# Kernel tuning notes

Hardware: AMD Instinct MI355X
Metric: run time of the kernel (lower is better)

Reference implementation:

```python
import jax, jax.numpy as jnp
import numpy as np

B, N, D, H = 32, 2048, 1024, 16
HD = D // H


def setup_inputs() -> dict:
    key = jax.random.key(0)
    ks = jax.random.split(key, 12)
    s = 1.0 / np.sqrt(D)  # xavier-ish scale for square projections
    return {
        "z": jax.random.normal(ks[0], (B, N, D), dtype=jnp.float32),
        "mask": jax.random.bernoulli(ks[1], 0.9, (B, N)),
        "query": jax.random.normal(ks[2], (1, 1, D), dtype=jnp.float32) * s,
        "w_q": jax.random.normal(ks[3], (D, D), dtype=jnp.float32) * s,
        "w_k": jax.random.normal(ks[4], (D, D), dtype=jnp.float32) * s,
        "w_v": jax.random.normal(ks[5], (D, D), dtype=jnp.float32) * s,
        "b_q": jnp.zeros((D,), dtype=jnp.float32),
        "b_k": jnp.zeros((D,), dtype=jnp.float32),
        "b_v": jnp.zeros((D,), dtype=jnp.float32),
        "w_o": jax.random.normal(ks[6], (D, D), dtype=jnp.float32) * s,
        "b_o": jnp.zeros((D,), dtype=jnp.float32),
    }


def reference(z, mask, query, w_q, w_k, w_v, b_q, b_k, b_v, w_o, b_o):
    # mask: True = valid key. Guarantee at least one valid key per row
    # (torch code sets mask[b, 0] = True for all-False rows).
    all_false = ~jnp.any(mask, axis=1)                 # [B]
    valid = mask.at[:, 0].set(mask[:, 0] | all_false)  # [B, N]

    # Projections (PyTorch Linear: x @ W.T + b)
    q = (query @ w_q.T + b_q).reshape(H, HD)           # single shared query -> [H, HD]
    k = (z @ w_k.T + b_k).reshape(B, N, H, HD)
    v = (z @ w_v.T + b_v).reshape(B, N, H, HD)

    scale = 1.0 / jnp.sqrt(jnp.asarray(HD, dtype=z.dtype))
    scores = jnp.einsum('hd,bnhd->bhn', q, k) * scale  # [B, H, N]
    scores = jnp.where(valid[:, None, :], scores, -jnp.inf)
    attn = jax.nn.softmax(scores, axis=-1)             # [B, H, N]

    pooled = jnp.einsum('bhn,bnhd->bhd', attn, v).reshape(B, D)
    return pooled @ w_o.T + b_o                        # [B, D]
```

## Files before the change

### kernel.cpp

```cpp
#include <hip/hip_runtime.h>
#include <stdint.h>

#define B_ 32
#define N_ 2048
#define D_ 1024
#define H_ 16

typedef __attribute__((ext_vector_type(8))) short short8;
typedef __attribute__((ext_vector_type(4))) float f32x4;

__device__ __forceinline__ unsigned short f2bf(float x) {
    unsigned u = __float_as_uint(x);
    u += 0x7FFFu + ((u >> 16) & 1u);
    return (unsigned short)(u >> 16);
}
__device__ __forceinline__ float bfhi(unsigned u) { return __uint_as_float(u & 0xFFFF0000u); }
__device__ __forceinline__ float bflo(unsigned u) { return __uint_as_float(u << 16); }

__global__ __launch_bounds__(256) void gemv_k(const float* __restrict__ vec_base, int vdiv,
        const float* __restrict__ W, const float* __restrict__ bias,
        float* __restrict__ out, int nout, int mod) {
    __shared__ float vlds[1024];
    int bx = blockIdx.x, t = threadIdx.x;
    const float* vec = vec_base + (size_t)(bx / vdiv) * 1024;
    float* orow = out + (size_t)(bx / mod) * 1024;
    int j0 = (bx % mod) * nout;
    *(float4*)&vlds[4 * t] = *(const float4*)&vec[4 * t];
    __syncthreads();
    int w = t >> 6, l = t & 63;
    int per = nout >> 2;
    for (int s = 0; s < per; s++) {
        int j = j0 + w * per + s;
        const float4* Wr = (const float4*)(W + (size_t)j * 1024);
        float acc = 0.f;
        #pragma unroll
        for (int kk = 0; kk < 4; kk++) {
            float4 a = Wr[kk * 64 + l];
            float4 v = *(const float4*)&vlds[(kk * 64 + l) * 4];
            acc += a.x * v.x + a.y * v.y + a.z * v.z + a.w * v.w;
        }
        #pragma unroll
        for (int m = 32; m >= 1; m >>= 1) acc += __shfl_xor(acc, m, 64);
        if (l == 0) orow[j] = acc + bias[j];
    }
}

__global__ __launch_bounds__(256) void prep_k(const float* __restrict__ q,
        const float* __restrict__ wk, const int* __restrict__ mask,
        unsigned short* __restrict__ rAf, int* __restrict__ any_ws) {
    __shared__ float qh[64];
    __shared__ int wf[4];
    int bx = blockIdx.x, t = threadIdx.x;
    if (bx < 16) {
        int h = bx;
        if (t < 64) qh[t] = q[h * 64 + t];
        __syncthreads();
        float4 acc = make_float4(0.f, 0.f, 0.f, 0.f);
        const float4* wk4 = (const float4*)wk;
        for (int j = 0; j < 64; j++) {
            float qv = qh[j];
            float4 wv = wk4[(size_t)(h * 64 + j) * 256 + t];
            acc.x += qv * wv.x; acc.y += qv * wv.y;
            acc.z += qv * wv.z; acc.w += qv * wv.w;
        }
        const float scale = 0.125f;
        float av[4] = {acc.x * scale, acc.y * scale, acc.z * scale, acc.w * scale};
        #pragma unroll
        for (int dd = 0; dd < 4; dd++) {
            int d = 4 * t + dd;
            int i = d >> 5, g = (d >> 3) & 3, jj = d & 7;
            int lane = (g << 4) | h;
            rAf[(size_t)(i * 64 + lane) * 8 + jj] = f2bf(av[dd]);
        }
    } else {
        int b = bx - 16;
        int v = 0;
        for (int k = 0; k < 8; k++) v |= mask[b * N_ + k * 256 + t];
        unsigned long long bal = __ballot(v != 0);
        int w = t >> 6;
        if ((t & 63) == 0) wf[w] = (bal != 0ull) ? 1 : 0;
        __syncthreads();
        if (t == 0) any_ws[b] = wf[0] | wf[1] | wf[2] | wf[3];
    }
}

__global__ __launch_bounds__(256, 2) void main_k(const float* __restrict__ z,
        const int* __restrict__ mask, const int* __restrict__ any_ws,
        const unsigned short* __restrict__ rAf,
        unsigned short* __restrict__ ctx_ws, float* __restrict__ l_ws) {
    __shared__ unsigned short zt[16][1024];
    __shared__ float Cpart[4][16][16];
    __shared__ float E_lds[256];
    __shared__ float lred[256];
    int bx = blockIdx.x, t = threadIdx.x;
    int b = bx >> 5, c = bx & 31;
    int n0 = c * 64;
    int w = t >> 6, l = t & 63;
    int frow = l & 15, fquad = l >> 4;
    int eh = t & 15, en = t >> 4;
    int anyb = any_ws[b];
    const float4* zg4 = (const float4*)(z + (size_t)b * N_ * D_);
    const short8* rA8 = (const short8*)rAf;
    float4 ctx[16];
    #pragma unroll
    for (int h = 0; h < 16; h++) ctx[h] = make_float4(0.f, 0.f, 0.f, 0.f);
    float l_acc = 0.f;

    for (int it = 0; it < 4; it++) {
        int rbase = n0 + it * 16;
        #pragma unroll
        for (int k = 0; k < 16; k++) {
            float4 v = zg4[(size_t)(rbase + k) * 256 + t];
            ushort4 o;
            o.x = f2bf(v.x); o.y = f2bf(v.y); o.z = f2bf(v.z); o.w = f2bf(v.w);
            *(ushort4*)&zt[k][4 * t] = o;
        }
        __syncthreads();
        f32x4 acc = {0.f, 0.f, 0.f, 0.f};
        #pragma unroll
        for (int ib = 0; ib < 8; ib++) {
            int i = w * 8 + ib;
            short8 af = rA8[i * 64 + l];
            short8 bf = *(const short8*)&zt[frow][i * 32 + fquad * 8];
            acc = __builtin_amdgcn_mfma_f32_16x16x32_bf16(af, bf, acc, 0, 0, 0);
        }
        #pragma unroll
        for (int r = 0; r < 4; r++) Cpart[w][fquad * 4 + r][frow] = acc[r];
        __syncthreads();
        {
            float s = Cpart[0][eh][en] + Cpart[1][eh][en]
                    + Cpart[2][eh][en] + Cpart[3][eh][en];
            int gn = rbase + en;
            bool valid = (mask[b * N_ + gn] != 0) || (gn == 0 && anyb == 0);
            float e = valid ? __expf(s) : 0.f;
            E_lds[t] = e;
            l_acc += e;
        }
        __syncthreads();
        for (int r = 0; r < 16; r++) {
            float er[16];
            *(float4*)&er[0]  = *(const float4*)&E_lds[r * 16 + 0];
            *(float4*)&er[4]  = *(const float4*)&E_lds[r * 16 + 4];
            *(float4*)&er[8]  = *(const float4*)&E_lds[r * 16 + 8];
            *(float4*)&er[12] = *(const float4*)&E_lds[r * 16 + 12];
            uint2 p = *(const uint2*)&zt[r][4 * t];
            float z0 = bflo(p.x), z1 = bfhi(p.x), z2 = bflo(p.y), z3 = bfhi(p.y);
            #pragma unroll
            for (int h = 0; h < 16; h++) {
                float e = er[h];
                ctx[h].x += e * z0; ctx[h].y += e * z1;
                ctx[h].z += e * z2; ctx[h].w += e * z3;
            }
        }
        __syncthreads();
    }
    #pragma unroll
    for (int h = 0; h < 16; h++) {
        ushort4 o;
        o.x = f2bf(ctx[h].x); o.y = f2bf(ctx[h].y);
        o.z = f2bf(ctx[h].z); o.w = f2bf(ctx[h].w);
        *(ushort4*)&ctx_ws[((size_t)bx * 16 + h) * 1024 + 4 * t] = o;
    }
    lred[t] = l_acc;
    __syncthreads();
    if (t < 16) {
        float s = 0.f;
        #pragma unroll
        for (int ss = 0; ss < 16; ss++) s += lred[ss * 16 + t];
        l_ws[bx * 16 + t] = s;
    }
}

__global__ __launch_bounds__(256) void reduce_k(const unsigned short* __restrict__ ctx_ws,
        const float* __restrict__ l_ws, const float* __restrict__ z,
        float* __restrict__ ctxsum) {
    int o = blockIdx.x * 256 + threadIdx.x;
    int b = o >> 14, h = (o >> 10) & 15, d = o & 1023;
    float s = 0.f, L = 0.f;
    for (int c = 0; c < 32; c++) {
        int bx = b * 32 + c;
        unsigned short us = ctx_ws[((size_t)bx * 16 + h) * 1024 + d];
        s += bflo((unsigned)us);
        L += l_ws[bx * 16 + h];
    }
    float val;
    if (L > 0.f) val = s / L;
    else         val = z[((size_t)b * N_ + 0) * D_ + d];
    ctxsum[o] = val;
}

extern "C" void kernel_launch(void* const* d_in, const int* in_sizes, int n_in,
                              void* d_out, int out_size, void* d_ws, size_t ws_size,
                              hipStream_t stream) {
    const float* z     = (const float*)d_in[0];
    const int*   mask  = (const int*)d_in[1];
    const float* query = (const float*)d_in[2];
    const float* w_q   = (const float*)d_in[3];
    const float* w_k   = (const float*)d_in[4];
    const float* w_v   = (const float*)d_in[5];
    const float* b_q   = (const float*)d_in[6];
    const float* b_v   = (const float*)d_in[8];
    const float* w_o   = (const float*)d_in[9];
    const float* b_o   = (const float*)d_in[10];
    float* out = (float*)d_out;

    char* ws = (char*)d_ws;
    float*          q_ws   = (float*)(ws + 0);
    int*            any_ws = (int*)(ws + 4096);
    unsigned short* rAf    = (unsigned short*)(ws + 8192);
    float*          l_ws   = (float*)(ws + 40960);
    float*          ctxsum = (float*)(ws + 131072);
    float*          pooled = (float*)(ws + 2228224);
    unsigned short* ctx_ws = (unsigned short*)(ws + 4194304);

    gemv_k<<<64, 256, 0, stream>>>(query, 64, w_q, b_q, q_ws, 16, 64);
    prep_k<<<48, 256, 0, stream>>>(q_ws, w_k, mask, rAf, any_ws);
    main_k<<<1024, 256, 0, stream>>>(z, mask, any_ws, rAf, ctx_ws, l_ws);
    reduce_k<<<2048, 256, 0, stream>>>(ctx_ws, l_ws, z, ctxsum);
    gemv_k<<<512, 256, 0, stream>>>(ctxsum, 1, w_v, b_v, pooled, 64, 16);
    gemv_k<<<512, 256, 0, stream>>>(pooled, 16, w_o, b_o, out, 64, 16);
}
```

Measured before the change: 469.8 us.

## Double-buffer z tiles in main kernel and fuse reduction into w_v gemv

Main kernel now processes 128 rows per block with register prefetch of the next 16-row z tile overlapping the MFMA/accumulate work on the current LDS buffer. Partial contexts are written in fp32 and the cross-chunk reduction and normalization are fused into the w_v gemv, removing a kernel and a bf16 round trip. The q projection is folded into prep_k and the gemvs compute four outputs per pass. The added prefetch registers may raise register pressure and halve the block count.

New measurement: 733.2 us. +56.1%, slower.

```diff
diff --git a/kernel.cpp b/kernel.cpp
--- a/kernel.cpp
+++ b/kernel.cpp
@@ -17,51 +17,44 @@
 __device__ __forceinline__ float bfhi(unsigned u) { return __uint_as_float(u & 0xFFFF0000u); }
 __device__ __forceinline__ float bflo(unsigned u) { return __uint_as_float(u << 16); }
 
-__global__ __launch_bounds__(256) void gemv_k(const float* __restrict__ vec_base, int vdiv,
-        const float* __restrict__ W, const float* __restrict__ bias,
-        float* __restrict__ out, int nout, int mod) {
-    __shared__ float vlds[1024];
-    int bx = blockIdx.x, t = threadIdx.x;
-    const float* vec = vec_base + (size_t)(bx / vdiv) * 1024;
-    float* orow = out + (size_t)(bx / mod) * 1024;
-    int j0 = (bx % mod) * nout;
-    *(float4*)&vlds[4 * t] = *(const float4*)&vec[4 * t];
-    __syncthreads();
-    int w = t >> 6, l = t & 63;
-    int per = nout >> 2;
-    for (int s = 0; s < per; s++) {
-        int j = j0 + w * per + s;
-        const float4* Wr = (const float4*)(W + (size_t)j * 1024);
-        float acc = 0.f;
-        #pragma unroll
-        for (int kk = 0; kk < 4; kk++) {
-            float4 a = Wr[kk * 64 + l];
-            float4 v = *(const float4*)&vlds[(kk * 64 + l) * 4];
-            acc += a.x * v.x + a.y * v.y + a.z * v.z + a.w * v.w;
-        }
-        #pragma unroll
-        for (int m = 32; m >= 1; m >>= 1) acc += __shfl_xor(acc, m, 64);
-        if (l == 0) orow[j] = acc + bias[j];
-    }
-}
-
-__global__ __launch_bounds__(256) void prep_k(const float* __restrict__ q,
-        const float* __restrict__ wk, const int* __restrict__ mask,
+__global__ __launch_bounds__(256) void prep_k(const float* __restrict__ query,
+        const float* __restrict__ w_q, const float* __restrict__ b_q,
+        const float* __restrict__ w_k, const int* __restrict__ mask,
         unsigned short* __restrict__ rAf, int* __restrict__ any_ws) {
+    __shared__ __align__(16) float qv[1024];
+    __shared__ float qpart[64][4];
     __shared__ float qh[64];
     __shared__ int wf[4];
     int bx = blockIdx.x, t = threadIdx.x;
     if (bx < 16) {
         int h = bx;
-        if (t < 64) qh[t] = q[h * 64 + t];
+        *(float4*)&qv[4 * t] = *(const float4*)&query[4 * t];
+        __syncthreads();
+        {
+            int j = t >> 2, qr = t & 3;
+            const float4* wq4 = (const float4*)w_q;
+            const float4* qv4 = (const float4*)qv;
+            float a = 0.f;
+            #pragma unroll 4
+            for (int kk = 0; kk < 64; kk++) {
+                float4 wv = wq4[(size_t)(h * 64 + j) * 256 + qr * 64 + kk];
+                float4 vv = qv4[qr * 64 + kk];
+                a += wv.x * vv.x + wv.y * vv.y + wv.z * vv.z + wv.w * vv.w;
+            }
+            qpart[j][qr] = a;
+        }
+        __syncthreads();
+        if (t < 64)
+            qh[t] = qpart[t][0] + qpart[t][1] + qpart[t][2] + qpart[t][3] + b_q[h * 64 + t];
         __syncthreads();
         float4 acc = make_float4(0.f, 0.f, 0.f, 0.f);
-        const float4* wk4 = (const float4*)wk;
-        for (int j = 0; j < 64; j++) {
-            float qv = qh[j];
-            float4 wv = wk4[(size_t)(h * 64 + j) * 256 + t];
-            acc.x += qv * wv.x; acc.y += qv * wv.y;
-            acc.z += qv * wv.z; acc.w += qv * wv.w;
+        const float4* wk4 = (const float4*)w_k;
+        #pragma unroll 4
+        for (int jj = 0; jj < 64; jj++) {
+            float qq = qh[jj];
+            float4 wv = wk4[(size_t)(h * 64 + jj) * 256 + t];
+            acc.x += qq * wv.x; acc.y += qq * wv.y;
+            acc.z += qq * wv.z; acc.w += qq * wv.w;
         }
         const float scale = 0.125f;
         float av[4] = {acc.x * scale, acc.y * scale, acc.z * scale, acc.w * scale};
@@ -87,14 +80,14 @@
 __global__ __launch_bounds__(256, 2) void main_k(const float* __restrict__ z,
         const int* __restrict__ mask, const int* __restrict__ any_ws,
         const unsigned short* __restrict__ rAf,
-        unsigned short* __restrict__ ctx_ws, float* __restrict__ l_ws) {
-    __shared__ unsigned short zt[16][1024];
+        float* __restrict__ part, float* __restrict__ l_part) {
+    __shared__ __align__(16) unsigned short zt[2][16][1040];
     __shared__ float Cpart[4][16][16];
     __shared__ float E_lds[256];
     __shared__ float lred[256];
     int bx = blockIdx.x, t = threadIdx.x;
-    int b = bx >> 5, c = bx & 31;
-    int n0 = c * 64;
+    int b = bx >> 4, c = bx & 15;
+    int n0 = c * 128;
     int w = t >> 6, l = t & 63;
     int frow = l & 15, fquad = l >> 4;
     int eh = t & 15, en = t >> 4;
@@ -106,31 +99,40 @@
     for (int h = 0; h < 16; h++) ctx[h] = make_float4(0.f, 0.f, 0.f, 0.f);
     float l_acc = 0.f;
 
-    for (int it = 0; it < 4; it++) {
-        int rbase = n0 + it * 16;
-        #pragma unroll
-        for (int k = 0; k < 16; k++) {
-            float4 v = zg4[(size_t)(rbase + k) * 256 + t];
-            ushort4 o;
-            o.x = f2bf(v.x); o.y = f2bf(v.y); o.z = f2bf(v.z); o.w = f2bf(v.w);
-            *(ushort4*)&zt[k][4 * t] = o;
-        }
-        __syncthreads();
+    float4 vv[16];
+    #pragma unroll
+    for (int k = 0; k < 16; k++) vv[k] = zg4[(size_t)(n0 + k) * 256 + t];
+    #pragma unroll
+    for (int k = 0; k < 16; k++) {
+        ushort4 o;
+        o.x = f2bf(vv[k].x); o.y = f2bf(vv[k].y);
+        o.z = f2bf(vv[k].z); o.w = f2bf(vv[k].w);
+        *(ushort4*)&zt[0][k][4 * t] = o;
+    }
+
+    for (int it = 0; it < 8; it++) {
+        int p = it & 1;
+        __syncthreads();
+        if (it < 7) {
+            int rb = n0 + (it + 1) * 16;
+            #pragma unroll
+            for (int k = 0; k < 16; k++) vv[k] = zg4[(size_t)(rb + k) * 256 + t];
+        }
         f32x4 acc = {0.f, 0.f, 0.f, 0.f};
         #pragma unroll
         for (int ib = 0; ib < 8; ib++) {
             int i = w * 8 + ib;
             short8 af = rA8[i * 64 + l];
-            short8 bf = *(const short8*)&zt[frow][i * 32 + fquad * 8];
+            short8 bf = *(const short8*)&zt[p][frow][i * 32 + fquad * 8];
             acc = __builtin_amdgcn_mfma_f32_16x16x32_bf16(af, bf, acc, 0, 0, 0);
         }
         #pragma unroll
         for (int r = 0; r < 4; r++) Cpart[w][fquad * 4 + r][frow] = acc[r];
         __syncthreads();
         {
+            int gn = n0 + it * 16 + en;
             float s = Cpart[0][eh][en] + Cpart[1][eh][en]
                     + Cpart[2][eh][en] + Cpart[3][eh][en];
-            int gn = rbase + en;
             bool valid = (mask[b * N_ + gn] != 0) || (gn == 0 && anyb == 0);
             float e = valid ? __expf(s) : 0.f;
             E_lds[t] = e;
@@ -143,8 +145,8 @@
             *(float4*)&er[4]  = *(const float4*)&E_lds[r * 16 + 4];
             *(float4*)&er[8]  = *(const float4*)&E_lds[r * 16 + 8];
             *(float4*)&er[12] = *(const float4*)&E_lds[r * 16 + 12];
-            uint2 p = *(const uint2*)&zt[r][4 * t];
-            float z0 = bflo(p.x), z1 = bfhi(p.x), z2 = bflo(p.y), z3 = bfhi(p.y);
+            uint2 pz = *(const uint2*)&zt[p][r][4 * t];
+            float z0 = bflo(pz.x), z1 = bfhi(pz.x), z2 = bflo(pz.y), z3 = bfhi(pz.y);
             #pragma unroll
             for (int h = 0; h < 16; h++) {
                 float e = er[h];
@@ -152,41 +154,121 @@
                 ctx[h].z += e * z2; ctx[h].w += e * z3;
             }
         }
-        __syncthreads();
-    }
-    #pragma unroll
-    for (int h = 0; h < 16; h++) {
-        ushort4 o;
-        o.x = f2bf(ctx[h].x); o.y = f2bf(ctx[h].y);
-        o.z = f2bf(ctx[h].z); o.w = f2bf(ctx[h].w);
-        *(ushort4*)&ctx_ws[((size_t)bx * 16 + h) * 1024 + 4 * t] = o;
-    }
+        if (it < 7) {
+            #pragma unroll
+            for (int k = 0; k < 16; k++) {
+                ushort4 o;
+                o.x = f2bf(vv[k].x); o.y = f2bf(vv[k].y);
+                o.z = f2bf(vv[k].z); o.w = f2bf(vv[k].w);
+                *(ushort4*)&zt[p ^ 1][k][4 * t] = o;
+            }
+        }
+    }
+    #pragma unroll
+    for (int h = 0; h < 16; h++)
+        *(float4*)&part[((size_t)bx * 16 + h) * 1024 + 4 * t] = ctx[h];
     lred[t] = l_acc;
     __syncthreads();
     if (t < 16) {
         float s = 0.f;
         #pragma unroll
-        for (int ss = 0; ss < 16; ss++) s += lred[ss * 16 + t];
-        l_ws[bx * 16 + t] = s;
-    }
-}
-
-__global__ __launch_bounds__(256) void reduce_k(const unsigned short* __restrict__ ctx_ws,
-        const float* __restrict__ l_ws, const float* __restrict__ z,
-        float* __restrict__ ctxsum) {
-    int o = blockIdx.x * 256 + threadIdx.x;
-    int b = o >> 14, h = (o >> 10) & 15, d = o & 1023;
-    float s = 0.f, L = 0.f;
-    for (int c = 0; c < 32; c++) {
-        int bx = b * 32 + c;
-        unsigned short us = ctx_ws[((size_t)bx * 16 + h) * 1024 + d];
-        s += bflo((unsigned)us);
-        L += l_ws[bx * 16 + h];
-    }
-    float val;
-    if (L > 0.f) val = s / L;
-    else         val = z[((size_t)b * N_ + 0) * D_ + d];
-    ctxsum[o] = val;
+        for (int g = 0; g < 16; g++) s += lred[g * 16 + t];
+        l_part[bx * 16 + t] = s;
+    }
+}
+
+__global__ __launch_bounds__(256) void gemv_wv_k(const float* __restrict__ part,
+        const float* __restrict__ l_part, const float* __restrict__ w_v,
+        const float* __restrict__ b_v, float* __restrict__ pooled) {
+    __shared__ __align__(16) float vlds[1024];
+    int bx = blockIdx.x, t = threadIdx.x;
+    int b = bx >> 4, h = bx & 15;
+    float L = 0.f;
+    #pragma unroll
+    for (int cc = 0; cc < 16; cc++) L += l_part[(b * 16 + cc) * 16 + h];
+    float rL = 1.f / L;
+    float sx = 0.f, sy = 0.f, sz = 0.f, sw = 0.f;
+    #pragma unroll
+    for (int cc = 0; cc < 16; cc++) {
+        const float4* p4 = (const float4*)&part[(((size_t)(b * 16 + cc)) * 16 + h) * 1024];
+        float4 v = p4[t];
+        sx += v.x; sy += v.y; sz += v.z; sw += v.w;
+    }
+    float4 o = make_float4(sx * rL, sy * rL, sz * rL, sw * rL);
+    *(float4*)&vlds[4 * t] = o;
+    __syncthreads();
+    int w = t >> 6, l = t & 63;
+    const float4* v4 = (const float4*)vlds;
+    float* orow = pooled + (size_t)b * 1024;
+    #pragma unroll
+    for (int s0 = 0; s0 < 16; s0 += 4) {
+        int jb = h * 64 + w * 16 + s0;
+        float a0 = 0.f, a1 = 0.f, a2 = 0.f, a3 = 0.f;
+        #pragma unroll
+        for (int kk = 0; kk < 4; kk++) {
+            float4 v = v4[kk * 64 + l];
+            float4 w0 = *(const float4*)&w_v[(size_t)(jb + 0) * 1024 + (kk * 64 + l) * 4];
+            float4 w1 = *(const float4*)&w_v[(size_t)(jb + 1) * 1024 + (kk * 64 + l) * 4];
+            float4 w2 = *(const float4*)&w_v[(size_t)(jb + 2) * 1024 + (kk * 64 + l) * 4];
+            float4 w3 = *(const float4*)&w_v[(size_t)(jb + 3) * 1024 + (kk * 64 + l) * 4];
+            a0 += w0.x * v.x + w0.y * v.y + w0.z * v.z + w0.w * v.w;
+            a1 += w1.x * v.x + w1.y * v.y + w1.z * v.z + w1.w * v.w;
+            a2 += w2.x * v.x + w2.y * v.y + w2.z * v.z + w2.w * v.w;
+            a3 += w3.x * v.x + w3.y * v.y + w3.z * v.z + w3.w * v.w;
+        }
+        #pragma unroll
+        for (int m = 32; m >= 1; m >>= 1) {
+            a0 += __shfl_xor(a0, m, 64); a1 += __shfl_xor(a1, m, 64);
+            a2 += __shfl_xor(a2, m, 64); a3 += __shfl_xor(a3, m, 64);
+        }
+        if (l == 0) {
+            orow[jb + 0] = a0 + b_v[jb + 0];
+            orow[jb + 1] = a1 + b_v[jb + 1];
+            orow[jb + 2] = a2 + b_v[jb + 2];
+            orow[jb + 3] = a3 + b_v[jb + 3];
+        }
+    }
+}
+
+__global__ __launch_bounds__(256) void gemv_wo_k(const float* __restrict__ pooled,
+        const float* __restrict__ w_o, const float* __restrict__ b_o,
+        float* __restrict__ out) {
+    __shared__ __align__(16) float vlds[1024];
+    int bx = blockIdx.x, t = threadIdx.x;
+    int b = bx >> 4, q = bx & 15;
+    *(float4*)&vlds[4 * t] = *(const float4*)&pooled[(size_t)b * 1024 + 4 * t];
+    __syncthreads();
+    int w = t >> 6, l = t & 63;
+    const float4* v4 = (const float4*)vlds;
+    float* orow = out + (size_t)b * 1024;
+    #pragma unroll
+    for (int s0 = 0; s0 < 16; s0 += 4) {
+        int jb = q * 64 + w * 16 + s0;
+        float a0 = 0.f, a1 = 0.f, a2 = 0.f, a3 = 0.f;
+        #pragma unroll
+        for (int kk = 0; kk < 4; kk++) {
+            float4 v = v4[kk * 64 + l];
+            float4 w0 = *(const float4*)&w_o[(size_t)(jb + 0) * 1024 + (kk * 64 + l) * 4];
+            float4 w1 = *(const float4*)&w_o[(size_t)(jb + 1) * 1024 + (kk * 64 + l) * 4];
+            float4 w2 = *(const float4*)&w_o[(size_t)(jb + 2) * 1024 + (kk * 64 + l) * 4];
+            float4 w3 = *(const float4*)&w_o[(size_t)(jb + 3) * 1024 + (kk * 64 + l) * 4];
+            a0 += w0.x * v.x + w0.y * v.y + w0.z * v.z + w0.w * v.w;
+            a1 += w1.x * v.x + w1.y * v.y + w1.z * v.z + w1.w * v.w;
+            a2 += w2.x * v.x + w2.y * v.y + w2.z * v.z + w2.w * v.w;
+            a3 += w3.x * v.x + w3.y * v.y + w3.z * v.z + w3.w * v.w;
+        }
+        #pragma unroll
+        for (int m = 32; m >= 1; m >>= 1) {
+            a0 += __shfl_xor(a0, m, 64); a1 += __shfl_xor(a1, m, 64);
+            a2 += __shfl_xor(a2, m, 64); a3 += __shfl_xor(a3, m, 64);
+        }
+        if (l == 0) {
+            orow[jb + 0] = a0 + b_o[jb + 0];
+            orow[jb + 1] = a1 + b_o[jb + 1];
+            orow[jb + 2] = a2 + b_o[jb + 2];
+            orow[jb + 3] = a3 + b_o[jb + 3];
+        }
+    }
 }
 
 extern "C" void kernel_launch(void* const* d_in, const int* in_sizes, int n_in,
@@ -205,18 +287,14 @@
     float* out = (float*)d_out;
 
     char* ws = (char*)d_ws;
-    float*          q_ws   = (float*)(ws + 0);
-    int*            any_ws = (int*)(ws + 4096);
-    unsigned short* rAf    = (unsigned short*)(ws + 8192);
-    float*          l_ws   = (float*)(ws + 40960);
-    float*          ctxsum = (float*)(ws + 131072);
-    float*          pooled = (float*)(ws + 2228224);
-    unsigned short* ctx_ws = (unsigned short*)(ws + 4194304);
-
-    gemv_k<<<64, 256, 0, stream>>>(query, 64, w_q, b_q, q_ws, 16, 64);
-    prep_k<<<48, 256, 0, stream>>>(q_ws, w_k, mask, rAf, any_ws);
-    main_k<<<1024, 256, 0, stream>>>(z, mask, any_ws, rAf, ctx_ws, l_ws);
-    reduce_k<<<2048, 256, 0, stream>>>(ctx_ws, l_ws, z, ctxsum);
-    gemv_k<<<512, 256, 0, stream>>>(ctxsum, 1, w_v, b_v, pooled, 64, 16);
-    gemv_k<<<512, 256, 0, stream>>>(pooled, 16, w_o, b_o, out, 64, 16);
-}
+    unsigned short* rAf    = (unsigned short*)(ws + 0);
+    int*            any_ws = (int*)(ws + 32768);
+    float*          l_part = (float*)(ws + 65536);
+    float*          pooled = (float*)(ws + 131072);
+    float*          part   = (float*)(ws + 1048576);
+
+    prep_k<<<48, 256, 0, stream>>>(query, w_q, b_q, w_k, mask, rAf, any_ws);
+    main_k<<<512, 256, 0, stream>>>(z, mask, any_ws, rAf, part, l_part);
+    gemv_wv_k<<<512, 256, 0, stream>>>(part, l_part, w_v, b_v, pooled);
+    gemv_wo_k<<<512, 256, 0, stream>>>(pooled, w_o, b_o, out);
+}
```
